# Optimization experiments

Measured on AMD Instinct MI355X. Metric: run time of the kernel, lower is better.

The kernel has to match this reference:

```python
import jax, jax.numpy as jnp
import numpy as np

EMBED_DIM = 1024
NUM_HEADS = 16
HEAD_DIM = EMBED_DIM // NUM_HEADS
SCALING = HEAD_DIM ** -0.5


def setup_inputs() -> dict:
    key = jax.random.key(0)
    ks = jax.random.split(key, 11)
    B, S, E = 4, 2048, EMBED_DIM
    s = 1.0 / np.sqrt(E)
    return {
        "query": jax.random.normal(ks[0], (B, S, E), jnp.float32),
        "key": jax.random.normal(ks[1], (B, S, E), jnp.float32),
        "value": jax.random.normal(ks[2], (B, S, E), jnp.float32),
        "q_w": jax.random.normal(ks[3], (E, E), jnp.float32) * s,
        "q_b": jax.random.normal(ks[4], (E,), jnp.float32) * 0.01,
        "k_w": jax.random.normal(ks[5], (E, E), jnp.float32) * s,
        "k_b": jax.random.normal(ks[6], (E,), jnp.float32) * 0.01,
        "v_w": jax.random.normal(ks[7], (E, E), jnp.float32) * s,
        "v_b": jax.random.normal(ks[8], (E,), jnp.float32) * 0.01,
        "out_w": jax.random.normal(ks[9], (E, E), jnp.float32) * s,
        "out_b": jax.random.normal(ks[10], (E,), jnp.float32) * 0.01,
    }


def reference(query, key, value, q_w, q_b, k_w, k_b, v_w, v_b, out_w, out_b):
    B, S, E = query.shape
    H, D = NUM_HEADS, HEAD_DIM
    # torch Linear: x @ W.T + b
    q = (query @ q_w.T + q_b).reshape(B, S, H, D).transpose(0, 2, 1, 3)  # [B,H,S,D]
    k = (key @ k_w.T + k_b).reshape(B, -1, H, D).transpose(0, 2, 1, 3)
    v = (value @ v_w.T + v_b).reshape(B, -1, H, D).transpose(0, 2, 1, 3)
    attn_scores = jnp.einsum("bhsd,bhtd->bhst", q, k) * SCALING  # [B,H,S,S]
    attn_weights = jax.nn.softmax(attn_scores, axis=-1)
    attn_output = jnp.einsum("bhst,bhtd->bhsd", attn_weights, v)
    attn_output = attn_output.transpose(0, 2, 1, 3).reshape(B, S, E)
    return attn_output @ out_w.T + out_b
```

## Files before the change

kernel.cpp:

```cpp
#include <hip/hip_runtime.h>
#include <stdint.h>
#include <stddef.h>

#define BB 4
#define SS 2048
#define EE 1024
#define HH 16
#define DD 64
#define MTOT (BB * SS)

#define SOFTMAX_C (0.125f * 1.44269504088896340736f)

using bf16x8 = __attribute__((ext_vector_type(8))) __bf16;
using f32x4  = __attribute__((ext_vector_type(4))) float;

__device__ inline unsigned short f2bf(float f) {
    union { float f; uint32_t u; } v; v.f = f;
    uint32_t u = v.u;
    u += 0x7fffu + ((u >> 16) & 1u);
    return (unsigned short)(u >> 16);
}

__device__ inline uint32_t packbf_trunc(float lo, float hi) {
    union { float f; uint32_t u; } a, b; a.f = lo; b.f = hi;
    return (a.u >> 16) | (b.u & 0xFFFF0000u);
}

__device__ inline void gld_lds16(const unsigned short* g, unsigned short* l) {
    __builtin_amdgcn_global_load_lds(
        (const __attribute__((address_space(1))) unsigned int*)g,
        (__attribute__((address_space(3))) unsigned int*)l,
        16, 0, 0);
}

__global__ __launch_bounds__(256) void cast3_f32_bf16(
    const float* __restrict__ a, const float* __restrict__ b,
    const float* __restrict__ c,
    unsigned short* __restrict__ oa, unsigned short* __restrict__ ob,
    unsigned short* __restrict__ oc, int n4) {
    int i = blockIdx.x * 256 + threadIdx.x;
    const float* src = (blockIdx.y == 0) ? a : (blockIdx.y == 1) ? b : c;
    unsigned short* dst = (blockIdx.y == 0) ? oa : (blockIdx.y == 1) ? ob : oc;
    if (i < n4) {
        float4 f = ((const float4*)src)[i];
        ushort4 o;
        o.x = f2bf(f.x); o.y = f2bf(f.y); o.z = f2bf(f.z); o.w = f2bf(f.w);
        ((ushort4*)dst)[i] = o;
    }
}

__global__ __launch_bounds__(256) void cast4_f32_bf16(
    const float* __restrict__ a, const float* __restrict__ b,
    const float* __restrict__ c, const float* __restrict__ d,
    unsigned short* __restrict__ oa, unsigned short* __restrict__ ob,
    unsigned short* __restrict__ oc, unsigned short* __restrict__ od, int n4) {
    int i = blockIdx.x * 256 + threadIdx.x;
    const float* src = (blockIdx.y == 0) ? a : (blockIdx.y == 1) ? b
                     : (blockIdx.y == 2) ? c : d;
    unsigned short* dst = (blockIdx.y == 0) ? oa : (blockIdx.y == 1) ? ob
                        : (blockIdx.y == 2) ? oc : od;
    if (i < n4) {
        float4 f = ((const float4*)src)[i];
        ushort4 o;
        o.x = f2bf(f.x); o.y = f2bf(f.y); o.z = f2bf(f.z); o.w = f2bf(f.w);
        ((ushort4*)dst)[i] = o;
    }
}

template <int MODE>
__global__ __launch_bounds__(256) void gemm_nt(
    const unsigned short* __restrict__ A,
    const unsigned short* __restrict__ W,
    const float* __restrict__ bias,
    void* __restrict__ outp, float oscale) {
    __shared__ __align__(16) unsigned short As[128 * 64];
    __shared__ __align__(16) unsigned short Bs[128 * 64];

    const int tid  = threadIdx.x;
    const int lane = tid & 63;
    const int wid  = tid >> 6;
    const int wm   = wid >> 1;
    const int wn   = wid & 1;
    const int quad = lane >> 4;
    const int l16  = lane & 15;
    const int m0   = blockIdx.y * 128;
    const int n0   = blockIdx.x * 128;

    f32x4 acc[4][4];
#pragma unroll
    for (int i = 0; i < 4; i++)
#pragma unroll
        for (int j = 0; j < 4; j++) acc[i][j] = (f32x4){0.f, 0.f, 0.f, 0.f};

    const int lrow = lane >> 3;
    const int lcol = (lane & 7) * 8;
    const unsigned short* ga = A + (size_t)(m0 + wid * 32 + lrow) * 1024 + lcol;
    const unsigned short* gb = W + (size_t)(n0 + wid * 32 + lrow) * 1024 + lcol;
    unsigned short* la = As + wid * 32 * 64;
    unsigned short* lb = Bs + wid * 32 * 64;

    for (int k0 = 0; k0 < 1024; k0 += 64) {
        __syncthreads();
#pragma unroll
        for (int c = 0; c < 4; c++) {
            gld_lds16(ga + (size_t)c * 8 * 1024 + k0, la + c * 8 * 64);
            gld_lds16(gb + (size_t)c * 8 * 1024 + k0, lb + c * 8 * 64);
        }
        __syncthreads();

#pragma unroll
        for (int kt = 0; kt < 2; kt++) {
            bf16x8 a[4], b[4];
#pragma unroll
            for (int mt = 0; mt < 4; mt++)
                a[mt] = *(const bf16x8*)(As + (wm * 64 + mt * 16 + l16) * 64 + kt * 32 + quad * 8);
#pragma unroll
            for (int nt = 0; nt < 4; nt++)
                b[nt] = *(const bf16x8*)(Bs + (wn * 64 + nt * 16 + l16) * 64 + kt * 32 + quad * 8);
#pragma unroll
            for (int mt = 0; mt < 4; mt++)
#pragma unroll
                for (int nt = 0; nt < 4; nt++)
                    acc[mt][nt] = __builtin_amdgcn_mfma_f32_16x16x32_bf16(
                        a[mt], b[nt], acc[mt][nt], 0, 0, 0);
        }
    }

#pragma unroll
    for (int mt = 0; mt < 4; mt++) {
#pragma unroll
        for (int nt = 0; nt < 4; nt++) {
            int gcol = n0 + wn * 64 + nt * 16 + l16;
            float bv = bias[gcol];
#pragma unroll
            for (int r = 0; r < 4; r++) {
                int grow = m0 + wm * 64 + mt * 16 + quad * 4 + r;
                float v = (acc[mt][nt][r] + bv) * oscale;
                if (MODE == 0) {
                    int bb = grow >> 11, sr = grow & 2047;
                    int hh = gcol >> 6,  dd = gcol & 63;
                    ((unsigned short*)outp)[(((size_t)(bb * HH + hh)) * SS + sr) * DD + dd] = f2bf(v);
                } else if (MODE == 2) {
                    int bb = grow >> 11, sr = grow & 2047;
                    int hh = gcol >> 6,  dd = gcol & 63;
                    ((unsigned short*)outp)[(((size_t)(bb * HH + hh)) * DD + dd) * SS + sr] = f2bf(v);
                } else {
                    ((float*)outp)[(size_t)grow * 1024 + gcol] = v;
                }
            }
        }
    }
}

__global__ __launch_bounds__(256) void flash_attn4(
    const unsigned short* __restrict__ Qh,
    const unsigned short* __restrict__ Kh,
    const unsigned short* __restrict__ Vtg,
    unsigned short* __restrict__ attn) {
    constexpr int LS = 72;
    __shared__ __align__(16) unsigned short Sh[128 * LS];
    __shared__ __align__(16) unsigned short Ps[8][16 * LS];
    unsigned short* Ks = Sh;
    unsigned short* Vs = Sh + 64 * LS;

    const int tid  = threadIdx.x;
    const int lane = tid & 63;
    const int w    = tid >> 6;
    const int quad = lane >> 4;
    const int l16  = lane & 15;
    const int bh   = blockIdx.y;
    const int q0   = blockIdx.x * 128;
    const size_t base = (size_t)bh * SS * DD;

    union { unsigned short u[8]; bf16x8 v; } onesu;
#pragma unroll
    for (int i = 0; i < 8; i++) onesu.u[i] = 0x3F80;
    const bf16x8 ones = onesu.v;

    bf16x8 bq[2][2];
#pragma unroll
    for (int s = 0; s < 2; s++)
#pragma unroll
        for (int kt = 0; kt < 2; kt++)
            bq[s][kt] = *(const bf16x8*)(Qh + base +
                (size_t)(q0 + w * 32 + s * 16 + l16) * DD + kt * 32 + quad * 8);

    f32x4 oT[2][4];
    f32x4 lacc[2];
#pragma unroll
    for (int s = 0; s < 2; s++) {
        lacc[s] = (f32x4){0.f, 0.f, 0.f, 0.f};
#pragma unroll
        for (int dt = 0; dt < 4; dt++) oT[s][dt] = (f32x4){0.f, 0.f, 0.f, 0.f};
    }

    for (int j0 = 0; j0 < SS; j0 += 64) {
        __syncthreads();
#pragma unroll
        for (int i = 0; i < 2; i++) {
            int c = tid + 256 * i;
            int row = c >> 3, col8 = (c & 7) * 8;
            *(uint4*)(Ks + row * LS + col8) =
                *(const uint4*)(Kh + base + (size_t)(j0 + row) * DD + col8);
            *(uint4*)(Vs + row * LS + col8) =
                *(const uint4*)(Vtg + base + (size_t)row * SS + j0 + col8);
        }
        __syncthreads();

        f32x4 sacc[2][4];
#pragma unroll
        for (int s = 0; s < 2; s++)
#pragma unroll
            for (int mt = 0; mt < 4; mt++) sacc[s][mt] = (f32x4){0.f, 0.f, 0.f, 0.f};
#pragma unroll
        for (int kt = 0; kt < 2; kt++) {
            bf16x8 ak[4];
#pragma unroll
            for (int mt = 0; mt < 4; mt++)
                ak[mt] = *(const bf16x8*)(Ks + (mt * 16 + l16) * LS + kt * 32 + quad * 8);
#pragma unroll
            for (int s = 0; s < 2; s++)
#pragma unroll
                for (int mt = 0; mt < 4; mt++)
                    sacc[s][mt] = __builtin_amdgcn_mfma_f32_16x16x32_bf16(
                        ak[mt], bq[s][kt], sacc[s][mt], 0, 0, 0);
        }

#pragma unroll
        for (int s = 0; s < 2; s++) {
#pragma unroll
            for (int mt = 0; mt < 4; mt++) {
                float p0 = __builtin_amdgcn_exp2f(sacc[s][mt][0]);
                float p1 = __builtin_amdgcn_exp2f(sacc[s][mt][1]);
                float p2 = __builtin_amdgcn_exp2f(sacc[s][mt][2]);
                float p3 = __builtin_amdgcn_exp2f(sacc[s][mt][3]);
                uint2 pk;
                pk.x = packbf_trunc(p0, p1);
                pk.y = packbf_trunc(p2, p3);
                *(uint2*)(&Ps[w * 2 + s][l16 * LS + mt * 16 + quad * 4]) = pk;
            }
        }

#pragma unroll
        for (int kt = 0; kt < 2; kt++) {
            bf16x8 av[4];
#pragma unroll
            for (int dt = 0; dt < 4; dt++)
                av[dt] = *(const bf16x8*)(Vs + (dt * 16 + l16) * LS + kt * 32 + quad * 8);
#pragma unroll
            for (int s = 0; s < 2; s++) {
                bf16x8 bp = *(const bf16x8*)(&Ps[w * 2 + s][l16 * LS + kt * 32 + quad * 8]);
#pragma unroll
                for (int dt = 0; dt < 4; dt++)
                    oT[s][dt] = __builtin_amdgcn_mfma_f32_16x16x32_bf16(
                        av[dt], bp, oT[s][dt], 0, 0, 0);
                lacc[s] = __builtin_amdgcn_mfma_f32_16x16x32_bf16(
                    ones, bp, lacc[s], 0, 0, 0);
            }
        }
    }

    float inv_l[2];
#pragma unroll
    for (int s = 0; s < 2; s++) inv_l[s] = 1.f / lacc[s][0];

    __syncthreads();
#pragma unroll
    for (int s = 0; s < 2; s++)
#pragma unroll
        for (int dt = 0; dt < 4; dt++)
#pragma unroll
            for (int r = 0; r < 4; r++)
                Sh[(w * 32 + s * 16 + l16) * LS + dt * 16 + quad * 4 + r] =
                    f2bf(oT[s][dt][r] * inv_l[s]);
    __syncthreads();

    const int b = bh >> 4, h = bh & 15;
#pragma unroll
    for (int i = 0; i < 4; i++) {
        int c = tid + 256 * i;
        int row = c >> 3, col8 = (c & 7) * 8;
        *(uint4*)(attn + ((size_t)b * SS + q0 + row) * EE + h * 64 + col8) =
            *(const uint4*)(Sh + row * LS + col8);
    }
}

extern "C" void kernel_launch(void* const* d_in, const int* in_sizes, int n_in,
                              void* d_out, int out_size, void* d_ws, size_t ws_size,
                              hipStream_t stream) {
    (void)in_sizes; (void)n_in; (void)out_size; (void)ws_size;
    const float* q_in  = (const float*)d_in[0];
    const float* k_in  = (const float*)d_in[1];
    const float* v_in  = (const float*)d_in[2];
    const float* q_w   = (const float*)d_in[3];
    const float* q_b   = (const float*)d_in[4];
    const float* k_w   = (const float*)d_in[5];
    const float* k_b   = (const float*)d_in[6];
    const float* v_w   = (const float*)d_in[7];
    const float* v_b   = (const float*)d_in[8];
    const float* out_w = (const float*)d_in[9];
    const float* out_b = (const float*)d_in[10];

    const size_t NX = (size_t)MTOT * EE;
    const size_t NW = (size_t)EE * EE;

    unsigned short* xq = (unsigned short*)d_ws;
    unsigned short* xk = xq + NX;
    unsigned short* xv = xk + NX;
    unsigned short* wq = xv + NX;
    unsigned short* wk = wq + NW;
    unsigned short* wv = wk + NW;
    unsigned short* wo = wv + NW;
    unsigned short* qh = wo + NW;
    unsigned short* kh = qh + NX;
    unsigned short* vt = kh + NX;
    unsigned short* attn = vt + NX;

    cast3_f32_bf16<<<dim3((int)(NX / 4 / 256), 3), 256, 0, stream>>>(
        q_in, k_in, v_in, xq, xk, xv, (int)(NX / 4));
    cast4_f32_bf16<<<dim3((int)(NW / 4 / 256), 4), 256, 0, stream>>>(
        q_w, k_w, v_w, out_w, wq, wk, wv, wo, (int)(NW / 4));

    dim3 ggrid(EE / 128, MTOT / 128);
    gemm_nt<0><<<ggrid, 256, 0, stream>>>(xq, wq, q_b, qh, SOFTMAX_C);
    gemm_nt<0><<<ggrid, 256, 0, stream>>>(xk, wk, k_b, kh, 1.0f);
    gemm_nt<2><<<ggrid, 256, 0, stream>>>(xv, wv, v_b, vt, 1.0f);

    flash_attn4<<<dim3(SS / 128, BB * HH), 256, 0, stream>>>(qh, kh, vt, attn);

    gemm_nt<1><<<ggrid, 256, 0, stream>>>(attn, wo, out_b, (float*)d_out, 1.0f);
}
```

Before: 421.1 us.

## Keep softmax probabilities in registers and compute V projection transposed

The attention kernel stops staging exponentiated probabilities through shared memory. It uses the register layout of the 16x16x16 bf16 MFMA directly as the B operand for the PV product and the row-sum, which removes the LDS round trip. The V projection GEMM now runs with its operands swapped, W·Xᵀ, so the transposed V output is written with contiguous sequence-dimension stores instead of strided ones. The cost is using the older K=16 MFMA, which issues twice as many instructions for the same work as the K=32 form.

```diff
diff --git a/kernel.cpp b/kernel.cpp
--- a/kernel.cpp
+++ b/kernel.cpp
@@ -13,6 +13,7 @@
 
 using bf16x8 = __attribute__((ext_vector_type(8))) __bf16;
 using f32x4  = __attribute__((ext_vector_type(4))) float;
+using s16x4  = __attribute__((ext_vector_type(4))) short;
 
 __device__ inline unsigned short f2bf(float f) {
     union { float f; uint32_t u; } v; v.f = f;
@@ -131,18 +132,19 @@
 #pragma unroll
         for (int nt = 0; nt < 4; nt++) {
             int gcol = n0 + wn * 64 + nt * 16 + l16;
-            float bv = bias[gcol];
+            float bvn = (MODE != 3) ? bias[gcol] : 0.f;
 #pragma unroll
             for (int r = 0; r < 4; r++) {
                 int grow = m0 + wm * 64 + mt * 16 + quad * 4 + r;
+                float bv = (MODE == 3) ? bias[grow] : bvn;
                 float v = (acc[mt][nt][r] + bv) * oscale;
                 if (MODE == 0) {
                     int bb = grow >> 11, sr = grow & 2047;
                     int hh = gcol >> 6,  dd = gcol & 63;
                     ((unsigned short*)outp)[(((size_t)(bb * HH + hh)) * SS + sr) * DD + dd] = f2bf(v);
-                } else if (MODE == 2) {
-                    int bb = grow >> 11, sr = grow & 2047;
-                    int hh = gcol >> 6,  dd = gcol & 63;
+                } else if (MODE == 3) {
+                    int bb = gcol >> 11, sr = gcol & 2047;
+                    int hh = grow >> 6,  dd = grow & 63;
                     ((unsigned short*)outp)[(((size_t)(bb * HH + hh)) * DD + dd) * SS + sr] = f2bf(v);
                 } else {
                     ((float*)outp)[(size_t)grow * 1024 + gcol] = v;
@@ -152,14 +154,13 @@
     }
 }
 
-__global__ __launch_bounds__(256) void flash_attn4(
+__global__ __launch_bounds__(256) void flash_attn5(
     const unsigned short* __restrict__ Qh,
     const unsigned short* __restrict__ Kh,
     const unsigned short* __restrict__ Vtg,
     unsigned short* __restrict__ attn) {
     constexpr int LS = 72;
     __shared__ __align__(16) unsigned short Sh[128 * LS];
-    __shared__ __align__(16) unsigned short Ps[8][16 * LS];
     unsigned short* Ks = Sh;
     unsigned short* Vs = Sh + 64 * LS;
 
@@ -172,10 +173,10 @@
     const int q0   = blockIdx.x * 128;
     const size_t base = (size_t)bh * SS * DD;
 
-    union { unsigned short u[8]; bf16x8 v; } onesu;
-#pragma unroll
-    for (int i = 0; i < 8; i++) onesu.u[i] = 0x3F80;
-    const bf16x8 ones = onesu.v;
+    union { unsigned short u[4]; s16x4 v; } onesu;
+#pragma unroll
+    for (int i = 0; i < 4; i++) onesu.u[i] = 0x3F80;
+    const s16x4 ones = onesu.v;
 
     bf16x8 bq[2][2];
 #pragma unroll
@@ -226,6 +227,7 @@
                         ak[mt], bq[s][kt], sacc[s][mt], 0, 0, 0);
         }
 
+        s16x4 bpf[2][4];
 #pragma unroll
         for (int s = 0; s < 2; s++) {
 #pragma unroll
@@ -234,28 +236,24 @@
                 float p1 = __builtin_amdgcn_exp2f(sacc[s][mt][1]);
                 float p2 = __builtin_amdgcn_exp2f(sacc[s][mt][2]);
                 float p3 = __builtin_amdgcn_exp2f(sacc[s][mt][3]);
-                uint2 pk;
-                pk.x = packbf_trunc(p0, p1);
-                pk.y = packbf_trunc(p2, p3);
-                *(uint2*)(&Ps[w * 2 + s][l16 * LS + mt * 16 + quad * 4]) = pk;
+                union { uint32_t w[2]; s16x4 v; } pk;
+                pk.w[0] = packbf_trunc(p0, p1);
+                pk.w[1] = packbf_trunc(p2, p3);
+                bpf[s][mt] = pk.v;
+                lacc[s] = __builtin_amdgcn_mfma_f32_16x16x16bf16_1k(
+                    ones, pk.v, lacc[s], 0, 0, 0);
             }
         }
 
 #pragma unroll
-        for (int kt = 0; kt < 2; kt++) {
-            bf16x8 av[4];
-#pragma unroll
-            for (int dt = 0; dt < 4; dt++)
-                av[dt] = *(const bf16x8*)(Vs + (dt * 16 + l16) * LS + kt * 32 + quad * 8);
-#pragma unroll
-            for (int s = 0; s < 2; s++) {
-                bf16x8 bp = *(const bf16x8*)(&Ps[w * 2 + s][l16 * LS + kt * 32 + quad * 8]);
-#pragma unroll
-                for (int dt = 0; dt < 4; dt++)
-                    oT[s][dt] = __builtin_amdgcn_mfma_f32_16x16x32_bf16(
-                        av[dt], bp, oT[s][dt], 0, 0, 0);
-                lacc[s] = __builtin_amdgcn_mfma_f32_16x16x32_bf16(
-                    ones, bp, lacc[s], 0, 0, 0);
+        for (int mt = 0; mt < 4; mt++) {
+#pragma unroll
+            for (int dt = 0; dt < 4; dt++) {
+                s16x4 av = *(const s16x4*)(Vs + (dt * 16 + l16) * LS + mt * 16 + quad * 4);
+#pragma unroll
+                for (int s = 0; s < 2; s++)
+                    oT[s][dt] = __builtin_amdgcn_mfma_f32_16x16x16bf16_1k(
+                        av, bpf[s][mt], oT[s][dt], 0, 0, 0);
             }
         }
     }
@@ -322,11 +320,12 @@
         q_w, k_w, v_w, out_w, wq, wk, wv, wo, (int)(NW / 4));
 
     dim3 ggrid(EE / 128, MTOT / 128);
+    dim3 ggridT(MTOT / 128, EE / 128);
     gemm_nt<0><<<ggrid, 256, 0, stream>>>(xq, wq, q_b, qh, SOFTMAX_C);
     gemm_nt<0><<<ggrid, 256, 0, stream>>>(xk, wk, k_b, kh, 1.0f);
-    gemm_nt<2><<<ggrid, 256, 0, stream>>>(xv, wv, v_b, vt, 1.0f);
-
-    flash_attn4<<<dim3(SS / 128, BB * HH), 256, 0, stream>>>(qh, kh, vt, attn);
+    gemm_nt<3><<<ggridT, 256, 0, stream>>>(wv, xv, v_b, vt, 1.0f);
+
+    flash_attn5<<<dim3(SS / 128, BB * HH), 256, 0, stream>>>(qh, kh, vt, attn);
 
     gemm_nt<1><<<ggrid, 256, 0, stream>>>(attn, wo, out_b, (float*)d_out, 1.0f);
 }
```

Result: faster. 412.6 us (-2.0%).
